# Kernel tuning notes

Measured on AMD Instinct MI355X. Metric: run time of the kernel, lower is better.

Reference implementation:

```python
import jax, jax.numpy as jnp
import numpy as np

NEG_SLOPE = 0.01  # torch nn.LeakyReLU default


def setup_inputs() -> dict:
    key = jax.random.key(0)
    k1, k2, k3 = jax.random.split(key, 3)
    B, V, T, F = 64, 64, 256, 64
    X = jax.random.normal(k1, (B, V, T), dtype=jnp.float32)
    A = jax.random.normal(k2, (T, V, V), dtype=jnp.float32)   # learnable_adj
    W = jax.random.normal(k3, (F, 1), dtype=jnp.float32)      # linear weight [out, in=1], no bias
    return {"X": X, "A": A, "W": W}


def reference(X, A, W):
    # X: [B, V, T], A: [T, V, V], W: [F, 1]
    B, V, T = X.shape
    eye = jnp.eye(V, dtype=A.dtype)
    # adj_t = sigmoid(A_t) * (1 - I) + I, batched over all timesteps at once
    adj = jax.nn.sigmoid(A) * (1.0 - eye) + eye               # [T, V, V]
    Xp = jnp.transpose(X, (0, 2, 1))                          # [B, T, V]
    # H_agg[b,t,v] = sum_w adj[t,v,w] * X[b,t,w]  (adj @ X_t with X_t as [V,1])
    H_agg = jnp.einsum('tvw,btw->btv', adj, Xp)               # [B, T, V]
    # Linear(in=1, out=F, no bias): H_out[b,t,v,f] = H_agg[b,t,v] * W[f,0]
    H = H_agg[..., None] * W[:, 0]                            # [B, T, V, F]
    H = jnp.where(H >= 0, H, NEG_SLOPE * H)                   # LeakyReLU
    return H.reshape(B, T, -1)                                # [B, T, V*F]
```

## Files before the change

### kernel.cpp

```cpp
#include <hip/hip_runtime.h>

#define BB 64
#define VV 64
#define TT 256
#define FF 64
constexpr float NEG_SLOPE = 0.01f;

__global__ __launch_bounds__(256) void gnn_fused(
    const float* __restrict__ X,
    const float* __restrict__ A,
    const float* __restrict__ W,
    float* __restrict__ out)
{
    __shared__ float adjS[VV][VV + 1];
    __shared__ float xs[VV];
    __shared__ float hs[VV];

    const int tid = threadIdx.x;
    const int bid = blockIdx.x;
    const int t = bid / BB;
    const int b = bid % BB;

    const float* At = A + (size_t)t * (VV * VV);
    #pragma unroll
    for (int i = 0; i < (VV * VV) / 256; ++i) {
        int idx = i * 256 + tid;
        int v = idx >> 6;
        int w = idx & 63;
        float a = At[idx];
        float s = 1.0f / (1.0f + __expf(-a));
        adjS[v][w] = (v == w) ? 1.0f : s;
    }

    if (tid < VV) {
        xs[tid] = X[(size_t)b * (VV * TT) + (size_t)tid * TT + t];
    }
    __syncthreads();

    {
        const int v = tid >> 2;
        const int part = tid & 3;
        float sum = 0.0f;
        #pragma unroll
        for (int i = 0; i < 16; ++i) {
            int w = part * 16 + i;
            sum += adjS[v][w] * xs[w];
        }
        sum += __shfl_xor(sum, 1);
        sum += __shfl_xor(sum, 2);
        if (part == 0) hs[v] = sum;
    }
    __syncthreads();

    const float4 w4 = *reinterpret_cast<const float4*>(W + ((4 * tid) & 63));
    float4* out4 = reinterpret_cast<float4*>(
        out + (size_t)(b * TT + t) * (VV * FF));
    #pragma unroll
    for (int k = 0; k < 4; ++k) {
        int idx4 = k * 256 + tid;
        float h = hs[idx4 >> 4];
        float4 r;
        r.x = h * w4.x;
        r.y = h * w4.y;
        r.z = h * w4.z;
        r.w = h * w4.w;
        r.x = (r.x >= 0.0f) ? r.x : NEG_SLOPE * r.x;
        r.y = (r.y >= 0.0f) ? r.y : NEG_SLOPE * r.y;
        r.z = (r.z >= 0.0f) ? r.z : NEG_SLOPE * r.z;
        r.w = (r.w >= 0.0f) ? r.w : NEG_SLOPE * r.w;
        out4[idx4] = r;
    }
}

extern "C" void kernel_launch(void* const* d_in, const int* in_sizes, int n_in,
                              void* d_out, int out_size, void* d_ws, size_t ws_size,
                              hipStream_t stream) {
    const float* X = (const float*)d_in[0];
    const float* A = (const float*)d_in[1];
    const float* W = (const float*)d_in[2];
    float* out = (float*)d_out;

    gnn_fused<<<BB * TT, 256, 0, stream>>>(X, A, W, out);
}
```

Baseline: 295.4 us.

## Split into per-timestep aggregation kernel and separate output expansion kernel

The fused kernel recomputed the sigmoid adjacency matrix for every (batch, timestep) block, reloading 16KB of A and evaluating 4096 exponentials 64 times per timestep. The work is now split in two kernels. The first, with one block per timestep, builds the adjacency once and computes H for all batches from LDS into a workspace buffer. The second is a purely bandwidth-bound kernel that expands H by W and applies LeakyReLU. The cost is an extra launch, a round trip for a 4MB intermediate, and strided gathers of X in the aggregation kernel.

```diff
diff --git a/kernel.cpp b/kernel.cpp
--- a/kernel.cpp
+++ b/kernel.cpp
@@ -6,20 +6,16 @@
 #define FF 64
 constexpr float NEG_SLOPE = 0.01f;
 
-__global__ __launch_bounds__(256) void gnn_fused(
+__global__ __launch_bounds__(256) void gnn_agg(
     const float* __restrict__ X,
     const float* __restrict__ A,
-    const float* __restrict__ W,
-    float* __restrict__ out)
+    float* __restrict__ H)
 {
     __shared__ float adjS[VV][VV + 1];
-    __shared__ float xs[VV];
-    __shared__ float hs[VV];
+    __shared__ float xsS[VV][VV + 1];
 
     const int tid = threadIdx.x;
-    const int bid = blockIdx.x;
-    const int t = bid / BB;
-    const int b = bid % BB;
+    const int t = blockIdx.x;
 
     const float* At = A + (size_t)t * (VV * VV);
     #pragma unroll
@@ -32,29 +28,46 @@
         adjS[v][w] = (v == w) ? 1.0f : s;
     }
 
-    if (tid < VV) {
-        xs[tid] = X[(size_t)b * (VV * TT) + (size_t)tid * TT + t];
+    #pragma unroll
+    for (int i = 0; i < (VV * VV) / 256; ++i) {
+        int idx = i * 256 + tid;
+        int b = idx >> 6;
+        int w = idx & 63;
+        xsS[b][w] = X[(size_t)b * (VV * TT) + (size_t)w * TT + t];
     }
     __syncthreads();
 
-    {
-        const int v = tid >> 2;
-        const int part = tid & 3;
+    #pragma unroll
+    for (int i = 0; i < 16; ++i) {
+        int flat = i * 256 + tid;
+        int b = flat >> 6;
+        int v = flat & 63;
         float sum = 0.0f;
         #pragma unroll
-        for (int i = 0; i < 16; ++i) {
-            int w = part * 16 + i;
-            sum += adjS[v][w] * xs[w];
+        for (int w = 0; w < VV; ++w) {
+            sum += adjS[v][w] * xsS[b][w];
         }
-        sum += __shfl_xor(sum, 1);
-        sum += __shfl_xor(sum, 2);
-        if (part == 0) hs[v] = sum;
+        H[(size_t)b * (TT * VV) + (size_t)t * VV + v] = sum;
     }
+}
+
+__global__ __launch_bounds__(256) void gnn_expand(
+    const float* __restrict__ H,
+    const float* __restrict__ W,
+    float* __restrict__ out)
+{
+    __shared__ float hs[VV];
+
+    const int tid = threadIdx.x;
+    const int bid = blockIdx.x;
+
+    if (tid < VV) {
+        hs[tid] = H[(size_t)bid * VV + tid];
+    }
+    const float4 w4 = *reinterpret_cast<const float4*>(W + ((4 * tid) & 63));
     __syncthreads();
 
-    const float4 w4 = *reinterpret_cast<const float4*>(W + ((4 * tid) & 63));
-    float4* out4 = reinterpret_cast<float4*>(
-        out + (size_t)(b * TT + t) * (VV * FF));
+    float4* out4 = reinterpret_cast<float4*>(out + (size_t)bid * (VV * FF));
     #pragma unroll
     for (int k = 0; k < 4; ++k) {
         int idx4 = k * 256 + tid;
@@ -79,6 +92,8 @@
     const float* A = (const float*)d_in[1];
     const float* W = (const float*)d_in[2];
     float* out = (float*)d_out;
+    float* H = (float*)d_ws;
 
-    gnn_fused<<<BB * TT, 256, 0, stream>>>(X, A, W, out);
+    gnn_agg<<<TT, 256, 0, stream>>>(X, A, H);
+    gnn_expand<<<BB * TT, 256, 0, stream>>>(H, W, out);
 }
```

After: 307.9 us. 1.04x slower.
